# Optimization experiments

Measured on AMD Instinct MI355X. Metric: run time of the kernel, lower is better.

Reference implementation:

```python
import jax, jax.numpy as jnp
import numpy as np

N = 20000      # nodes
E = 320000     # edges (before self-loops)
IN = 256       # in_channels
HID = 64       # hidden_channels
HEADS = 4      # num_heads
OUT = 64       # out_channels
NEG_SLOPE = 0.2  # GATConv default leaky-relu slope


def setup_inputs() -> dict:
    key = jax.random.key(0)
    ks = jax.random.split(key, 12)
    s = 0.1
    x = jax.random.normal(ks[0], (N, IN), dtype=jnp.float32)
    edge_index = jax.random.randint(ks[1], (2, E), 0, N, dtype=jnp.int64)
    # Layer 1: IN -> HID per head, HEADS heads, concat
    W1 = jax.random.normal(ks[2], (IN, HEADS * HID), dtype=jnp.float32) * s
    a1_src = jax.random.normal(ks[3], (HEADS, HID), dtype=jnp.float32) * s
    a1_dst = jax.random.normal(ks[4], (HEADS, HID), dtype=jnp.float32) * s
    b1 = jnp.zeros((HEADS * HID,), dtype=jnp.float32)
    # Layer 2: HEADS*HID -> OUT, 1 head, no concat
    W2 = jax.random.normal(ks[5], (HEADS * HID, OUT), dtype=jnp.float32) * s
    a2_src = jax.random.normal(ks[6], (1, OUT), dtype=jnp.float32) * s
    a2_dst = jax.random.normal(ks[7], (1, OUT), dtype=jnp.float32) * s
    b2 = jnp.zeros((OUT,), dtype=jnp.float32)
    return {"x": x, "edge_index": edge_index,
            "W1": W1, "a1_src": a1_src, "a1_dst": a1_dst, "b1": b1,
            "W2": W2, "a2_src": a2_src, "a2_dst": a2_dst, "b2": b2}


def _gat_layer(x, src, dst, W, a_src, a_dst, bias, heads, out_c, concat):
    n = x.shape[0]
    h = (x @ W).reshape(n, heads, out_c)                    # [N,H,C]
    e_src = jnp.einsum('nhc,hc->nh', h, a_src)              # [N,H]
    e_dst = jnp.einsum('nhc,hc->nh', h, a_dst)              # [N,H]
    logits = jax.nn.leaky_relu(e_src[src] + e_dst[dst], NEG_SLOPE)  # [E',H]
    # segment softmax over incoming edges of each dst node
    m = jax.ops.segment_max(logits, dst, num_segments=n)    # [N,H]
    p = jnp.exp(logits - m[dst])                            # [E',H]
    z = jax.ops.segment_sum(p, dst, num_segments=n)         # [N,H]
    alpha = p / z[dst]                                      # [E',H]
    out = jax.ops.segment_sum(h[src] * alpha[:, :, None], dst, num_segments=n)
    out = out.reshape(n, heads * out_c) if concat else out.mean(axis=1)
    return out + bias


def reference(x, edge_index, W1, a1_src, a1_dst, b1, W2, a2_src, a2_dst, b2):
    # PyG GATConv adds self-loops by default
    loop = jnp.arange(N, dtype=edge_index.dtype)
    src = jnp.concatenate([edge_index[0], loop])
    dst = jnp.concatenate([edge_index[1], loop])
    h = _gat_layer(x, src, dst, W1, a1_src, a1_dst, b1, HEADS, HID, True)
    h = jax.nn.elu(h)
    # F.dropout defaults training=False -> identity in eval reference
    out = _gat_layer(h, src, dst, W2, a2_src, a2_dst, b2, 1, OUT, False)
    return out
```

## Files before the change

### kernel.cpp

```cpp
#include <hip/hip_runtime.h>
#include <math.h>

#define NEG 0.2f
#define CSTRIDE 64
#define LOG2E 1.4426950408889634f

typedef __attribute__((ext_vector_type(8))) short bf16x8;
typedef __attribute__((ext_vector_type(4))) float f32x4;
typedef unsigned int u32;

__device__ inline float bf2f(unsigned short u) {
    union { unsigned int i; float f; } v; v.i = ((unsigned int)u) << 16; return v.f;
}
__device__ inline unsigned short f2bf(float f) {
    union { float f; unsigned int i; } v; v.f = f;
    unsigned int r = v.i + 0x7FFF + ((v.i >> 16) & 1);
    return (unsigned short)(r >> 16);
}
__device__ inline void unpack8(uint4 hv, float* o) {
    o[0] = bf2f((unsigned short)(hv.x & 0xffffu));
    o[1] = bf2f((unsigned short)(hv.x >> 16));
    o[2] = bf2f((unsigned short)(hv.y & 0xffffu));
    o[3] = bf2f((unsigned short)(hv.y >> 16));
    o[4] = bf2f((unsigned short)(hv.z & 0xffffu));
    o[5] = bf2f((unsigned short)(hv.z >> 16));
    o[6] = bf2f((unsigned short)(hv.w & 0xffffu));
    o[7] = bf2f((unsigned short)(hv.w >> 16));
}
__device__ inline void load_lds16(const unsigned short* g, unsigned short* l) {
    __builtin_amdgcn_global_load_lds((const __attribute__((address_space(1))) u32*)g,
                                     (__attribute__((address_space(3))) u32*)l, 16, 0, 0);
}

__device__ void gemm1_block(int bm, int bn, unsigned short* As, unsigned short* Bs,
                            const unsigned short* __restrict__ A,
                            const unsigned short* __restrict__ Bt,
                            unsigned short* __restrict__ C,
                            const float* __restrict__ a1s, const float* __restrict__ a1d,
                            float* __restrict__ es, float* __restrict__ ed, int M) {
    const int tid = threadIdx.x;
    const int wave = tid >> 6, lane = tid & 63;
    const int wm = (wave >> 1) * 64, wn = (wave & 1) * 64;
    const int lm = lane & 15, kq = lane >> 4;
    const int rA = lane >> 2, cA = (lane & 3) * 8;

    int grA[2], grB[2];
#pragma unroll
    for (int i = 0; i < 2; ++i) {
        int c = wave * 2 + i;
        int gr = bm + c * 16 + rA;
        if (gr >= M) gr = M - 1;
        grA[i] = gr;
        grB[i] = bn + c * 16 + rA;
    }

    auto stage = [&](int t, int b) {
        const int k0 = t * 32;
        const int ka = (k0 < 512) ? k0 : k0 - 512;
#pragma unroll
        for (int i = 0; i < 2; ++i) {
            int c = wave * 2 + i;
            load_lds16(A + (size_t)grA[i] * 512 + ka + cA, As + b * 4096 + c * 512);
            load_lds16(Bt + (size_t)grB[i] * 768 + k0 + cA, Bs + b * 4096 + c * 512);
        }
    };

    f32x4 acc[4][4] = {};
    stage(0, 0);
    stage(1, 1);
    int buf = 0;
    for (int t = 0; t < 24; ++t) {
        if (t < 22) {
            int nb = buf + 2;
            if (nb >= 3) nb -= 3;
            stage(t + 2, nb);
            asm volatile("s_waitcnt vmcnt(8)" ::: "memory");
        } else if (t == 22) {
            asm volatile("s_waitcnt vmcnt(4)" ::: "memory");
        } else {
            asm volatile("s_waitcnt vmcnt(0)" ::: "memory");
        }
        __builtin_amdgcn_s_barrier();
        __builtin_amdgcn_sched_barrier(0);
        bf16x8 af[4], bfr[4];
#pragma unroll
        for (int f = 0; f < 4; ++f) af[f] = *(const bf16x8*)(As + buf * 4096 + (wm + f * 16 + lm) * 32 + kq * 8);
#pragma unroll
        for (int f = 0; f < 4; ++f) bfr[f] = *(const bf16x8*)(Bs + buf * 4096 + (wn + f * 16 + lm) * 32 + kq * 8);
#pragma unroll
        for (int fr = 0; fr < 4; ++fr)
#pragma unroll
            for (int fc = 0; fc < 4; ++fc)
                acc[fr][fc] = __builtin_amdgcn_mfma_f32_16x16x32_bf16(af[fr], bfr[fc], acc[fr][fc], 0, 0, 0);
        __builtin_amdgcn_s_barrier();
        __builtin_amdgcn_sched_barrier(0);
        buf = (buf + 1 == 3) ? 0 : buf + 1;
    }
    const int head = (bn + wn) >> 6;
    float asv[4], adv[4];
#pragma unroll
    for (int fc = 0; fc < 4; ++fc) {
        int ch = fc * 16 + lm;
        asv[fc] = a1s[head * 64 + ch];
        adv[fc] = a1d[head * 64 + ch];
    }
#pragma unroll
    for (int fr = 0; fr < 4; ++fr)
#pragma unroll
        for (int i = 0; i < 4; ++i) {
            int row = bm + wm + fr * 16 + kq * 4 + i;
            float se = 0.f, de = 0.f;
#pragma unroll
            for (int fc = 0; fc < 4; ++fc) {
                float c = acc[fr][fc][i];
                se = fmaf(asv[fc], c, se);
                de = fmaf(adv[fc], c, de);
            }
#pragma unroll
            for (int off = 1; off < 16; off <<= 1) {
                se += __shfl_xor(se, off, 64);
                de += __shfl_xor(de, off, 64);
            }
            if (row < M) {
                if (lm == 0) {
                    es[row * 4 + head] = se * LOG2E;
                    ed[row * 4 + head] = de * LOG2E;
                }
#pragma unroll
                for (int fc = 0; fc < 4; ++fc)
                    C[(size_t)row * 256 + bn + wn + fc * 16 + lm] = f2bf(acc[fr][fc][i]);
            }
        }
}

__global__ __launch_bounds__(256) void pre(const float* __restrict__ x,
                                           const float* __restrict__ W1,
                                           const float* __restrict__ W2,
                                           unsigned short* __restrict__ xs,
                                           unsigned short* __restrict__ Wt1,
                                           unsigned short* __restrict__ Wt2,
                                           int* __restrict__ cnt,
                                           int xb, int wb, int N) {
    int b = blockIdx.x, tid = threadIdx.x;
    if (b < xb) {
        int i = b * 256 + tid;
        if (i >= N * 64) return;
        int e0 = i * 4;
        int node = e0 >> 8, c = e0 & 255;
        float4 f = *(const float4*)(x + e0);
        unsigned short h0 = f2bf(f.x), h1 = f2bf(f.y), h2 = f2bf(f.z), h3 = f2bf(f.w);
        uint2 hi, lo;
        hi.x = (u32)h0 | ((u32)h1 << 16);
        hi.y = (u32)h2 | ((u32)h3 << 16);
        lo.x = (u32)f2bf(f.x - bf2f(h0)) | ((u32)f2bf(f.y - bf2f(h1)) << 16);
        lo.y = (u32)f2bf(f.z - bf2f(h2)) | ((u32)f2bf(f.w - bf2f(h3)) << 16);
        *(uint2*)(xs + (size_t)node * 512 + c) = hi;
        *(uint2*)(xs + (size_t)node * 512 + 256 + c) = lo;
    } else if (b < xb + wb) {
        int i = (b - xb) * 256 + tid;
        const float* W;
        unsigned short* Wt;
        int outc;
        if (i < 256 * 768) { W = W1; Wt = Wt1; outc = 256; }
        else {
            i -= 256 * 768;
            if (i >= 64 * 768) return;
            W = W2; Wt = Wt2; outc = 64;
        }
        int n = i & (outc - 1);
        int k = (outc == 256) ? (i >> 8) : (i >> 6);
        int ksrc = (k < 256) ? k : (k < 512 ? k - 256 : k - 512);
        float f = W[(size_t)ksrc * outc + n];
        unsigned short h = f2bf(f);
        if (k >= 512) h = f2bf(f - bf2f(h));
        Wt[(size_t)n * 768 + k] = h;
    } else {
        int i = (b - xb - wb) * 256 + tid;
        if (i < N) cnt[i] = 0;
    }
}

__global__ __launch_bounds__(256) void fused_g1fill(
    int gcnt,
    const unsigned short* __restrict__ A, const unsigned short* __restrict__ Bt,
    unsigned short* __restrict__ C,
    const float* __restrict__ a1s, const float* __restrict__ a1d,
    float* __restrict__ es, float* __restrict__ ed, int M,
    const int* __restrict__ ei, int E,
    int* __restrict__ cnt, int* __restrict__ csr) {
    __shared__ int uni[12288];
    if ((int)blockIdx.x < gcnt) {
        int gid = blockIdx.x;
        unsigned short* sm = (unsigned short*)uni;
        gemm1_block((gid >> 1) * 128, (gid & 1) * 128, sm, sm + 12288,
                    A, Bt, C, a1s, a1d, es, ed, M);
    } else {
        int e = (blockIdx.x - gcnt) * 256 + threadIdx.x;
        if (e < E + M) {
            int s, d;
            if (e < E) { s = ei[e]; d = ei[E + e]; }
            else       { s = d = e - E; }
            int c = atomicAdd(&cnt[d], 1);
            if (c < CSTRIDE) csr[(size_t)d * CSTRIDE + c] = s << 9;
        }
    }
}

__global__ __launch_bounds__(256) void gemm2_scores(const unsigned short* __restrict__ A,
                                                    const unsigned short* __restrict__ Bt,
                                                    unsigned short* __restrict__ C,
                                                    const float* __restrict__ a2s,
                                                    const float* __restrict__ a2d,
                                                    float* __restrict__ es,
                                                    float* __restrict__ ed, int M) {
    __shared__ unsigned short As[3][64 * 32];
    __shared__ unsigned short Bs[3][64 * 32];
    const int tid = threadIdx.x;
    const int bm = blockIdx.x * 64;
    const int wave = tid >> 6, lane = tid & 63;
    const int wm = wave * 16;
    const int lm = lane & 15, kq = lane >> 4;
    const int rA = lane >> 2, cA = (lane & 3) * 8;

    int grA = bm + wave * 16 + rA;
    if (grA >= M) grA = M - 1;
    int grB = wave * 16 + rA;

    auto stage = [&](int t, int b) {
        const int k0 = t * 32;
        const int ka = (k0 < 512) ? k0 : k0 - 512;
        load_lds16(A + (size_t)grA * 512 + ka + cA, &As[b][wave * 512]);
        load_lds16(Bt + (size_t)grB * 768 + k0 + cA, &Bs[b][wave * 512]);
    };

    f32x4 acc[4] = {};
    stage(0, 0);
    stage(1, 1);
    int buf = 0;
    for (int t = 0; t < 24; ++t) {
        if (t < 22) {
            int nb = buf + 2;
            if (nb >= 3) nb -= 3;
            stage(t + 2, nb);
            asm volatile("s_waitcnt vmcnt(4)" ::: "memory");
        } else if (t == 22) {
            asm volatile("s_waitcnt vmcnt(2)" ::: "memory");
        } else {
            asm volatile("s_waitcnt vmcnt(0)" ::: "memory");
        }
        __builtin_amdgcn_s_barrier();
        __builtin_amdgcn_sched_barrier(0);
        bf16x8 af = *(const bf16x8*)(&As[buf][(wm + lm) * 32 + kq * 8]);
        bf16x8 bfr[4];
#pragma unroll
        for (int f = 0; f < 4; ++f) bfr[f] = *(const bf16x8*)(&Bs[buf][(f * 16 + lm) * 32 + kq * 8]);
#pragma unroll
        for (int fc = 0; fc < 4; ++fc)
            acc[fc] = __builtin_amdgcn_mfma_f32_16x16x32_bf16(af, bfr[fc], acc[fc], 0, 0, 0);
        __builtin_amdgcn_s_barrier();
        __builtin_amdgcn_sched_barrier(0);
        buf = (buf + 1 == 3) ? 0 : buf + 1;
    }
    float asv[4], adv[4];
#pragma unroll
    for (int fc = 0; fc < 4; ++fc) {
        int ch = fc * 16 + lm;
        asv[fc] = a2s[ch];
        adv[fc] = a2d[ch];
    }
#pragma unroll
    for (int i = 0; i < 4; ++i) {
        int row = bm + wm + kq * 4 + i;
        float se = 0.f, de = 0.f;
#pragma unroll
        for (int fc = 0; fc < 4; ++fc) {
            float c = acc[fc][i];
            se = fmaf(asv[fc], c, se);
            de = fmaf(adv[fc], c, de);
        }
#pragma unroll
        for (int off = 1; off < 16; off <<= 1) {
            se += __shfl_xor(se, off, 64);
            de += __shfl_xor(de, off, 64);
        }
        if (row < M) {
            if (lm == 0) {
                es[row] = se * LOG2E;
                ed[row] = de * LOG2E;
            }
#pragma unroll
            for (int fc = 0; fc < 4; ++fc)
                C[(size_t)row * 64 + fc * 16 + lm] = f2bf(acc[fc][i]);
        }
    }
}

__global__ __launch_bounds__(256) void agg1(const unsigned short* __restrict__ h,
                                            const int* __restrict__ csr,
                                            const int* __restrict__ cnt,
                                            const float* __restrict__ es,
                                            const float* __restrict__ ed,
                                            const float* __restrict__ b1,
                                            unsigned short* __restrict__ outs, int n) {
    int node = blockIdx.x * 8 + (threadIdx.x >> 5);
    int g = threadIdx.x & 31;
    if (node >= n) return;
    int hh = g >> 3;
    int cb = g * 8;
    int cb2 = cb * 2;
    int hh4 = hh * 4;
    const char* hb = (const char*)h;
    const char* eb = (const char*)es;
    float edst = ed[node * 4 + hh];
    int j0 = node * CSTRIDE;
    int c0 = cnt[node];
    int j1 = j0 + (c0 < CSTRIDE ? c0 : CSTRIDE);
    float z0 = 0.f, z1 = 0.f, z2 = 0.f, z3 = 0.f;
    float a0[8] = {}, a1a[8] = {}, a2a[8] = {}, a3a[8] = {};
    int j = j0;
    for (; j + 4 <= j1; j += 4) {
        int o0 = csr[j], o1 = csr[j + 1], o2 = csr[j + 2], o3 = csr[j + 3];
        uint4 v0 = *(const uint4*)(hb + o0 + cb2);
        uint4 v1 = *(const uint4*)(hb + o1 + cb2);
        uint4 v2 = *(const uint4*)(hb + o2 + cb2);
        uint4 v3 = *(const uint4*)(hb + o3 + cb2);
        float l0 = *(const float*)(eb + (o0 >> 5) + hh4) + edst;
        float l1 = *(const float*)(eb + (o1 >> 5) + hh4) + edst;
        float l2 = *(const float*)(eb + (o2 >> 5) + hh4) + edst;
        float l3 = *(const float*)(eb + (o3 >> 5) + hh4) + edst;
        l0 = (l0 > 0.f) ? l0 : NEG * l0;
        l1 = (l1 > 0.f) ? l1 : NEG * l1;
        l2 = (l2 > 0.f) ? l2 : NEG * l2;
        l3 = (l3 > 0.f) ? l3 : NEG * l3;
        float p0 = exp2f(l0), p1 = exp2f(l1), p2 = exp2f(l2), p3 = exp2f(l3);
        z0 += p0; z1 += p1; z2 += p2; z3 += p3;
        float t[8];
        unpack8(v0, t);
#pragma unroll
        for (int c = 0; c < 8; ++c) a0[c] = fmaf(p0, t[c], a0[c]);
        unpack8(v1, t);
#pragma unroll
        for (int c = 0; c < 8; ++c) a1a[c] = fmaf(p1, t[c], a1a[c]);
        unpack8(v2, t);
#pragma unroll
        for (int c = 0; c < 8; ++c) a2a[c] = fmaf(p2, t[c], a2a[c]);
        unpack8(v3, t);
#pragma unroll
        for (int c = 0; c < 8; ++c) a3a[c] = fmaf(p3, t[c], a3a[c]);
    }
    for (; j < j1; ++j) {
        int o0 = csr[j];
        uint4 v0 = *(const uint4*)(hb + o0 + cb2);
        float l0 = *(const float*)(eb + (o0 >> 5) + hh4) + edst;
        l0 = (l0 > 0.f) ? l0 : NEG * l0;
        float p0 = exp2f(l0);
        z0 += p0;
        float t[8];
        unpack8(v0, t);
#pragma unroll
        for (int c = 0; c < 8; ++c) a0[c] = fmaf(p0, t[c], a0[c]);
    }
    float z = (z0 + z1) + (z2 + z3);
    float inv = 1.f / z;
    float r[8];
    unsigned short qh[8], ql[8];
#pragma unroll
    for (int c = 0; c < 8; ++c) {
        r[c] = ((a0[c] + a1a[c]) + (a2a[c] + a3a[c])) * inv + b1[cb + c];
        r[c] = (r[c] > 0.f) ? r[c] : (__expf(r[c]) - 1.f);
        qh[c] = f2bf(r[c]);
        ql[c] = f2bf(r[c] - bf2f(qh[c]));
    }
    uint4 hiw, low;
    hiw.x = (u32)qh[0] | ((u32)qh[1] << 16);
    hiw.y = (u32)qh[2] | ((u32)qh[3] << 16);
    hiw.z = (u32)qh[4] | ((u32)qh[5] << 16);
    hiw.w = (u32)qh[6] | ((u32)qh[7] << 16);
    low.x = (u32)ql[0] | ((u32)ql[1] << 16);
    low.y = (u32)ql[2] | ((u32)ql[3] << 16);
    low.z = (u32)ql[4] | ((u32)ql[5] << 16);
    low.w = (u32)ql[6] | ((u32)ql[7] << 16);
    *(uint4*)(outs + (size_t)node * 512 + cb) = hiw;
    *(uint4*)(outs + (size_t)node * 512 + 256 + cb) = low;
}

__global__ __launch_bounds__(256) void agg2(const unsigned short* __restrict__ h,
                                            const int* __restrict__ csr,
                                            const int* __restrict__ cnt,
                                            const float* __restrict__ es,
                                            const float* __restrict__ ed,
                                            const float* __restrict__ b2,
                                            float* __restrict__ out, int n) {
    int node = blockIdx.x * 32 + (threadIdx.x >> 3);
    int g = threadIdx.x & 7;
    if (node >= n) return;
    int cb = g * 8;
    int cb2 = cb * 2;
    const char* hb = (const char*)h;
    const char* eb = (const char*)es;
    float edst = ed[node];
    int j0 = node * CSTRIDE;
    int c0 = cnt[node];
    int j1 = j0 + (c0 < CSTRIDE ? c0 : CSTRIDE);
    float z0 = 0.f, z1 = 0.f, z2 = 0.f, z3 = 0.f;
    float a0[8] = {}, a1a[8] = {}, a2a[8] = {}, a3a[8] = {};
    int j = j0;
    for (; j + 4 <= j1; j += 4) {
        int o0 = csr[j], o1 = csr[j + 1], o2 = csr[j + 2], o3 = csr[j + 3];
        uint4 v0 = *(const uint4*)(hb + (o0 >> 2) + cb2);
        uint4 v1 = *(const uint4*)(hb + (o1 >> 2) + cb2);
        uint4 v2 = *(const uint4*)(hb + (o2 >> 2) + cb2);
        uint4 v3 = *(const uint4*)(hb + (o3 >> 2) + cb2);
        float l0 = *(const float*)(eb + (o0 >> 7)) + edst;
        float l1 = *(const float*)(eb + (o1 >> 7)) + edst;
        float l2 = *(const float*)(eb + (o2 >> 7)) + edst;
        float l3 = *(const float*)(eb + (o3 >> 7)) + edst;
        l0 = (l0 > 0.f) ? l0 : NEG * l0;
        l1 = (l1 > 0.f) ? l1 : NEG * l1;
        l2 = (l2 > 0.f) ? l2 : NEG * l2;
        l3 = (l3 > 0.f) ? l3 : NEG * l3;
        float p0 = exp2f(l0), p1 = exp2f(l1), p2 = exp2f(l2), p3 = exp2f(l3);
        z0 += p0; z1 += p1; z2 += p2; z3 += p3;
        float t[8];
        unpack8(v0, t);
#pragma unroll
        for (int c = 0; c < 8; ++c) a0[c] = fmaf(p0, t[c], a0[c]);
        unpack8(v1, t);
#pragma unroll
        for (int c = 0; c < 8; ++c) a1a[c] = fmaf(p1, t[c], a1a[c]);
        unpack8(v2, t);
#pragma unroll
        for (int c = 0; c < 8; ++c) a2a[c] = fmaf(p2, t[c], a2a[c]);
        unpack8(v3, t);
#pragma unroll
        for (int c = 0; c < 8; ++c) a3a[c] = fmaf(p3, t[c], a3a[c]);
    }
    for (; j < j1; ++j) {
        int o0 = csr[j];
        uint4 v0 = *(const uint4*)(hb + (o0 >> 2) + cb2);
        float l0 = *(const float*)(eb + (o0 >> 7)) + edst;
        l0 = (l0 > 0.f) ? l0 : NEG * l0;
        float p0 = exp2f(l0);
        z0 += p0;
        float t[8];
        unpack8(v0, t);
#pragma unroll
        for (int c = 0; c < 8; ++c) a0[c] = fmaf(p0, t[c], a0[c]);
    }
    float z = (z0 + z1) + (z2 + z3);
    float inv = 1.f / z;
    float4 r0, r1;
    r0.x = ((a0[0] + a1a[0]) + (a2a[0] + a3a[0])) * inv + b2[cb + 0];
    r0.y = ((a0[1] + a1a[1]) + (a2a[1] + a3a[1])) * inv + b2[cb + 1];
    r0.z = ((a0[2] + a1a[2]) + (a2a[2] + a3a[2])) * inv + b2[cb + 2];
    r0.w = ((a0[3] + a1a[3]) + (a2a[3] + a3a[3])) * inv + b2[cb + 3];
    r1.x = ((a0[4] + a1a[4]) + (a2a[4] + a3a[4])) * inv + b2[cb + 4];
    r1.y = ((a0[5] + a1a[5]) + (a2a[5] + a3a[5])) * inv + b2[cb + 5];
    r1.z = ((a0[6] + a1a[6]) + (a2a[6] + a3a[6])) * inv + b2[cb + 6];
    r1.w = ((a0[7] + a1a[7]) + (a2a[7] + a3a[7])) * inv + b2[cb + 7];
    *(float4*)(out + (size_t)node * 64 + cb) = r0;
    *(float4*)(out + (size_t)node * 64 + cb + 4) = r1;
}

extern "C" void kernel_launch(void* const* d_in, const int* in_sizes, int n_in,
                              void* d_out, int out_size, void* d_ws, size_t ws_size,
                              hipStream_t stream) {
    const float* x   = (const float*)d_in[0];
    const int*   ei  = (const int*)d_in[1];
    const float* W1  = (const float*)d_in[2];
    const float* a1s = (const float*)d_in[3];
    const float* a1d = (const float*)d_in[4];
    const float* b1  = (const float*)d_in[5];
    const float* W2  = (const float*)d_in[6];
    const float* a2s = (const float*)d_in[7];
    const float* a2d = (const float*)d_in[8];
    const float* b2  = (const float*)d_in[9];
    float* out = (float*)d_out;

    const int N = in_sizes[0] / 256;
    const int E = in_sizes[1] / 2;

    char* p = (char*)d_ws;
    auto take = [&](size_t bytes) {
        char* r = p;
        p += (bytes + 255) & ~(size_t)255;
        return r;
    };
    int* cnt  = (int*)take((size_t)N * 4);
    int* csr  = (int*)take((size_t)N * CSTRIDE * 4);
    unsigned short* hstk = (unsigned short*)take((size_t)N * 512 * 2);
    unsigned short* Wt1  = (unsigned short*)take((size_t)256 * 768 * 2);
    unsigned short* Wt2  = (unsigned short*)take((size_t)64 * 768 * 2);
    unsigned short* h1   = (unsigned short*)take((size_t)N * 256 * 2);
    unsigned short* h2   = (unsigned short*)take((size_t)N * 64 * 2);
    float* es1 = (float*)take((size_t)N * 4 * 4);
    float* ed1 = (float*)take((size_t)N * 4 * 4);
    float* es2 = (float*)take((size_t)N * 4);
    float* ed2 = (float*)take((size_t)N * 4);

    int xb = (N * 64 + 255) / 256;
    int wb = (256 * 768 + 64 * 768 + 255) / 256;
    int zb = (N + 255) / 256;
    pre<<<xb + wb + zb, 256, 0, stream>>>(x, W1, W2, hstk, Wt1, Wt2, cnt, xb, wb, N);

    int GT = 2 * ((N + 127) / 128);
    int eb = (E + N + 255) / 256;
    fused_g1fill<<<GT + eb, 256, 0, stream>>>(GT, hstk, Wt1, h1, a1s, a1d, es1, ed1, N,
                                              ei, E, cnt, csr);

    agg1<<<(N + 7) / 8, 256, 0, stream>>>(h1, csr, cnt, es1, ed1, b1, hstk, N);

    gemm2_scores<<<(N + 63) / 64, 256, 0, stream>>>(hstk, Wt2, h2, a2s, a2d, es2, ed2, N);

    agg2<<<(N + 31) / 32, 256, 0, stream>>>(h2, csr, cnt, es2, ed2, b2, out, N);
}
```

Before: 166.1 us.

## Fuse layer-1 aggregation into layer-2 GEMM kernel per 64-node tile

Merges agg1 and gemm2_scores into one kernel. Each block first aggregates its 64 destination nodes in 8 serial passes of 8 nodes and writes the ELU output (hi/lo bf16 split) to hstk. After a block barrier it runs the layer-2 GEMM and score computation on those same rows. This removes a kernel launch and the dependency gap between the two stages. In exchange the gather-bound aggregation now runs on about 313 blocks instead of about 2500, with passes serialized inside each block, so there is much less parallelism available to hide memory latency.

```diff
diff --git a/kernel.cpp b/kernel.cpp
--- a/kernel.cpp
+++ b/kernel.cpp
@@ -206,30 +206,123 @@
     }
 }
 
-__global__ __launch_bounds__(256) void gemm2_scores(const unsigned short* __restrict__ A,
-                                                    const unsigned short* __restrict__ Bt,
-                                                    unsigned short* __restrict__ C,
-                                                    const float* __restrict__ a2s,
-                                                    const float* __restrict__ a2d,
-                                                    float* __restrict__ es,
-                                                    float* __restrict__ ed, int M) {
+__global__ __launch_bounds__(256) void agg1_gemm2(
+    const unsigned short* __restrict__ h1, const int* __restrict__ csr,
+    const int* __restrict__ cnt,
+    const float* __restrict__ es1, const float* __restrict__ ed1,
+    const float* __restrict__ b1,
+    unsigned short* __restrict__ hstk,
+    const unsigned short* __restrict__ Bt,
+    unsigned short* __restrict__ h2,
+    const float* __restrict__ a2s, const float* __restrict__ a2d,
+    float* __restrict__ es2, float* __restrict__ ed2, int n) {
     __shared__ unsigned short As[3][64 * 32];
     __shared__ unsigned short Bs[3][64 * 32];
+    const int bm = blockIdx.x * 64;
+
+    {
+        int g = threadIdx.x & 31;
+        int grp = threadIdx.x >> 5;
+        int hh = g >> 3;
+        int cb = g * 8;
+        int cb2 = cb * 2;
+        int hh4 = hh * 4;
+        const char* hb = (const char*)h1;
+        const char* eb = (const char*)es1;
+#pragma unroll 1
+        for (int pass = 0; pass < 8; ++pass) {
+            int node = bm + pass * 8 + grp;
+            if (node < n) {
+                float edst = ed1[node * 4 + hh];
+                int j0 = node * CSTRIDE;
+                int c0 = cnt[node];
+                int j1 = j0 + (c0 < CSTRIDE ? c0 : CSTRIDE);
+                float z0 = 0.f, z1 = 0.f, z2 = 0.f, z3 = 0.f;
+                float a0[8] = {}, a1a[8] = {}, a2a[8] = {}, a3a[8] = {};
+                int j = j0;
+                for (; j + 4 <= j1; j += 4) {
+                    int o0 = csr[j], o1 = csr[j + 1], o2 = csr[j + 2], o3 = csr[j + 3];
+                    uint4 v0 = *(const uint4*)(hb + o0 + cb2);
+                    uint4 v1 = *(const uint4*)(hb + o1 + cb2);
+                    uint4 v2 = *(const uint4*)(hb + o2 + cb2);
+                    uint4 v3 = *(const uint4*)(hb + o3 + cb2);
+                    float l0 = *(const float*)(eb + (o0 >> 5) + hh4) + edst;
+                    float l1 = *(const float*)(eb + (o1 >> 5) + hh4) + edst;
+                    float l2 = *(const float*)(eb + (o2 >> 5) + hh4) + edst;
+                    float l3 = *(const float*)(eb + (o3 >> 5) + hh4) + edst;
+                    l0 = (l0 > 0.f) ? l0 : NEG * l0;
+                    l1 = (l1 > 0.f) ? l1 : NEG * l1;
+                    l2 = (l2 > 0.f) ? l2 : NEG * l2;
+                    l3 = (l3 > 0.f) ? l3 : NEG * l3;
+                    float p0 = exp2f(l0), p1 = exp2f(l1), p2 = exp2f(l2), p3 = exp2f(l3);
+                    z0 += p0; z1 += p1; z2 += p2; z3 += p3;
+                    float t[8];
+                    unpack8(v0, t);
+#pragma unroll
+                    for (int c = 0; c < 8; ++c) a0[c] = fmaf(p0, t[c], a0[c]);
+                    unpack8(v1, t);
+#pragma unroll
+                    for (int c = 0; c < 8; ++c) a1a[c] = fmaf(p1, t[c], a1a[c]);
+                    unpack8(v2, t);
+#pragma unroll
+                    for (int c = 0; c < 8; ++c) a2a[c] = fmaf(p2, t[c], a2a[c]);
+                    unpack8(v3, t);
+#pragma unroll
+                    for (int c = 0; c < 8; ++c) a3a[c] = fmaf(p3, t[c], a3a[c]);
+                }
+                for (; j < j1; ++j) {
+                    int o0 = csr[j];
+                    uint4 v0 = *(const uint4*)(hb + o0 + cb2);
+                    float l0 = *(const float*)(eb + (o0 >> 5) + hh4) + edst;
+                    l0 = (l0 > 0.f) ? l0 : NEG * l0;
+                    float p0 = exp2f(l0);
+                    z0 += p0;
+                    float t[8];
+                    unpack8(v0, t);
+#pragma unroll
+                    for (int c = 0; c < 8; ++c) a0[c] = fmaf(p0, t[c], a0[c]);
+                }
+                float z = (z0 + z1) + (z2 + z3);
+                float inv = 1.f / z;
+                float r[8];
+                unsigned short qh[8], ql[8];
+#pragma unroll
+                for (int c = 0; c < 8; ++c) {
+                    r[c] = ((a0[c] + a1a[c]) + (a2a[c] + a3a[c])) * inv + b1[cb + c];
+                    r[c] = (r[c] > 0.f) ? r[c] : (__expf(r[c]) - 1.f);
+                    qh[c] = f2bf(r[c]);
+                    ql[c] = f2bf(r[c] - bf2f(qh[c]));
+                }
+                uint4 hiw, low;
+                hiw.x = (u32)qh[0] | ((u32)qh[1] << 16);
+                hiw.y = (u32)qh[2] | ((u32)qh[3] << 16);
+                hiw.z = (u32)qh[4] | ((u32)qh[5] << 16);
+                hiw.w = (u32)qh[6] | ((u32)qh[7] << 16);
+                low.x = (u32)ql[0] | ((u32)ql[1] << 16);
+                low.y = (u32)ql[2] | ((u32)ql[3] << 16);
+                low.z = (u32)ql[4] | ((u32)ql[5] << 16);
+                low.w = (u32)ql[6] | ((u32)ql[7] << 16);
+                *(uint4*)(hstk + (size_t)node * 512 + cb) = hiw;
+                *(uint4*)(hstk + (size_t)node * 512 + 256 + cb) = low;
+            }
+        }
+    }
+    __syncthreads();
+
     const int tid = threadIdx.x;
-    const int bm = blockIdx.x * 64;
     const int wave = tid >> 6, lane = tid & 63;
     const int wm = wave * 16;
     const int lm = lane & 15, kq = lane >> 4;
     const int rA = lane >> 2, cA = (lane & 3) * 8;
 
     int grA = bm + wave * 16 + rA;
-    if (grA >= M) grA = M - 1;
+    if (grA >= n) grA = n - 1;
     int grB = wave * 16 + rA;
 
     auto stage = [&](int t, int b) {
         const int k0 = t * 32;
         const int ka = (k0 < 512) ? k0 : k0 - 512;
-        load_lds16(A + (size_t)grA * 512 + ka + cA, &As[b][wave * 512]);
+        load_lds16(hstk + (size_t)grA * 512 + ka + cA, &As[b][wave * 512]);
         load_lds16(Bt + (size_t)grB * 768 + k0 + cA, &Bs[b][wave * 512]);
     };
 
@@ -283,105 +376,16 @@
             se += __shfl_xor(se, off, 64);
             de += __shfl_xor(de, off, 64);
         }
-        if (row < M) {
+        if (row < n) {
             if (lm == 0) {
-                es[row] = se * LOG2E;
-                ed[row] = de * LOG2E;
+                es2[row] = se * LOG2E;
+                ed2[row] = de * LOG2E;
             }
 #pragma unroll
             for (int fc = 0; fc < 4; ++fc)
-                C[(size_t)row * 64 + fc * 16 + lm] = f2bf(acc[fc][i]);
-        }
-    }
-}
-
-__global__ __launch_bounds__(256) void agg1(const unsigned short* __restrict__ h,
-                                            const int* __restrict__ csr,
-                                            const int* __restrict__ cnt,
-                                            const float* __restrict__ es,
-                                            const float* __restrict__ ed,
-                                            const float* __restrict__ b1,
-                                            unsigned short* __restrict__ outs, int n) {
-    int node = blockIdx.x * 8 + (threadIdx.x >> 5);
-    int g = threadIdx.x & 31;
-    if (node >= n) return;
-    int hh = g >> 3;
-    int cb = g * 8;
-    int cb2 = cb * 2;
-    int hh4 = hh * 4;
-    const char* hb = (const char*)h;
-    const char* eb = (const char*)es;
-    float edst = ed[node * 4 + hh];
-    int j0 = node * CSTRIDE;
-    int c0 = cnt[node];
-    int j1 = j0 + (c0 < CSTRIDE ? c0 : CSTRIDE);
-    float z0 = 0.f, z1 = 0.f, z2 = 0.f, z3 = 0.f;
-    float a0[8] = {}, a1a[8] = {}, a2a[8] = {}, a3a[8] = {};
-    int j = j0;
-    for (; j + 4 <= j1; j += 4) {
-        int o0 = csr[j], o1 = csr[j + 1], o2 = csr[j + 2], o3 = csr[j + 3];
-        uint4 v0 = *(const uint4*)(hb + o0 + cb2);
-        uint4 v1 = *(const uint4*)(hb + o1 + cb2);
-        uint4 v2 = *(const uint4*)(hb + o2 + cb2);
-        uint4 v3 = *(const uint4*)(hb + o3 + cb2);
-        float l0 = *(const float*)(eb + (o0 >> 5) + hh4) + edst;
-        float l1 = *(const float*)(eb + (o1 >> 5) + hh4) + edst;
-        float l2 = *(const float*)(eb + (o2 >> 5) + hh4) + edst;
-        float l3 = *(const float*)(eb + (o3 >> 5) + hh4) + edst;
-        l0 = (l0 > 0.f) ? l0 : NEG * l0;
-        l1 = (l1 > 0.f) ? l1 : NEG * l1;
-        l2 = (l2 > 0.f) ? l2 : NEG * l2;
-        l3 = (l3 > 0.f) ? l3 : NEG * l3;
-        float p0 = exp2f(l0), p1 = exp2f(l1), p2 = exp2f(l2), p3 = exp2f(l3);
-        z0 += p0; z1 += p1; z2 += p2; z3 += p3;
-        float t[8];
-        unpack8(v0, t);
-#pragma unroll
-        for (int c = 0; c < 8; ++c) a0[c] = fmaf(p0, t[c], a0[c]);
-        unpack8(v1, t);
-#pragma unroll
-        for (int c = 0; c < 8; ++c) a1a[c] = fmaf(p1, t[c], a1a[c]);
-        unpack8(v2, t);
-#pragma unroll
-        for (int c = 0; c < 8; ++c) a2a[c] = fmaf(p2, t[c], a2a[c]);
-        unpack8(v3, t);
-#pragma unroll
-        for (int c = 0; c < 8; ++c) a3a[c] = fmaf(p3, t[c], a3a[c]);
-    }
-    for (; j < j1; ++j) {
-        int o0 = csr[j];
-        uint4 v0 = *(const uint4*)(hb + o0 + cb2);
-        float l0 = *(const float*)(eb + (o0 >> 5) + hh4) + edst;
-        l0 = (l0 > 0.f) ? l0 : NEG * l0;
-        float p0 = exp2f(l0);
-        z0 += p0;
-        float t[8];
-        unpack8(v0, t);
-#pragma unroll
-        for (int c = 0; c < 8; ++c) a0[c] = fmaf(p0, t[c], a0[c]);
-    }
-    float z = (z0 + z1) + (z2 + z3);
-    float inv = 1.f / z;
-    float r[8];
-    unsigned short qh[8], ql[8];
-#pragma unroll
-    for (int c = 0; c < 8; ++c) {
-        r[c] = ((a0[c] + a1a[c]) + (a2a[c] + a3a[c])) * inv + b1[cb + c];
-        r[c] = (r[c] > 0.f) ? r[c] : (__expf(r[c]) - 1.f);
-        qh[c] = f2bf(r[c]);
-        ql[c] = f2bf(r[c] - bf2f(qh[c]));
-    }
-    uint4 hiw, low;
-    hiw.x = (u32)qh[0] | ((u32)qh[1] << 16);
-    hiw.y = (u32)qh[2] | ((u32)qh[3] << 16);
-    hiw.z = (u32)qh[4] | ((u32)qh[5] << 16);
-    hiw.w = (u32)qh[6] | ((u32)qh[7] << 16);
-    low.x = (u32)ql[0] | ((u32)ql[1] << 16);
-    low.y = (u32)ql[2] | ((u32)ql[3] << 16);
-    low.z = (u32)ql[4] | ((u32)ql[5] << 16);
-    low.w = (u32)ql[6] | ((u32)ql[7] << 16);
-    *(uint4*)(outs + (size_t)node * 512 + cb) = hiw;
-    *(uint4*)(outs + (size_t)node * 512 + 256 + cb) = low;
+                h2[(size_t)row * 64 + fc * 16 + lm] = f2bf(acc[fc][i]);
+        }
+    }
 }
 
 __global__ __launch_bounds__(256) void agg2(const unsigned short* __restrict__ h,
@@ -508,9 +512,8 @@
     fused_g1fill<<<GT + eb, 256, 0, stream>>>(GT, hstk, Wt1, h1, a1s, a1d, es1, ed1, N,
                                               ei, E, cnt, csr);
 
-    agg1<<<(N + 7) / 8, 256, 0, stream>>>(h1, csr, cnt, es1, ed1, b1, hstk, N);
-
-    gemm2_scores<<<(N + 63) / 64, 256, 0, stream>>>(hstk, Wt2, h2, a2s, a2d, es2, ed2, N);
+    agg1_gemm2<<<(N + 63) / 64, 256, 0, stream>>>(h1, csr, cnt, es1, ed1, b1, hstk,
+                                                  Wt2, h2, a2s, a2d, es2, ed2, N);
 
     agg2<<<(N + 31) / 32, 256, 0, stream>>>(h2, csr, cnt, es2, ed2, b2, out, N);
 }
```

Measured after the change: 193.3 us. 16.4% more time.
